# Optimization experiments

Hardware: AMD Instinct MI355X
Metric: run time of the kernel (lower is better)

The kernel has to match this reference:

```python
import jax, jax.numpy as jnp
import numpy as np

M_, N_, L_, K_ = 8, 64, 4, 4
PT = 10.0
B_ = 512
CH = 128
FLAT = 64 * M_ * (N_ + 1)  # PhaseNet flatten size


def setup_inputs() -> dict:
    key = jax.random.key(0)
    ks = jax.random.split(key, 25)
    rn = lambda k, shape, s=1.0: jax.random.normal(k, shape, jnp.float32) * s
    W_SCALE = 0.05
    return {
        "x": rn(ks[0], (B_, L_, 2 * K_, M_, N_ + 1)),
        "H_re": rn(ks[1], (B_, M_, N_, L_, K_)),
        "H_im": rn(ks[2], (B_, M_, N_, L_, K_)),
        "ch_re": rn(ks[3], (B_, K_, M_)),
        "ch_im": rn(ks[4], (B_, K_, M_)),
        # PhaseNet params (1x1 convs stored as [out, in])
        "conv1_w": rn(ks[5], (64, 2 * K_), W_SCALE), "conv1_b": jnp.zeros((64,), jnp.float32),
        "conv2_w": rn(ks[6], (64, 64), W_SCALE), "conv2_b": jnp.zeros((64,), jnp.float32),
        "pl1_w": rn(ks[7], (4 * N_, FLAT), W_SCALE), "pl1_b": jnp.zeros((4 * N_,), jnp.float32),
        "pl2_w": rn(ks[8], (2 * N_, 4 * N_), W_SCALE), "pl2_b": jnp.zeros((2 * N_,), jnp.float32),
        # BeamNet params
        "b1_w": rn(ks[9], (CH, 2 * K_ * M_), W_SCALE), "b1_b": jnp.zeros((CH,), jnp.float32),
        "b2_w": rn(ks[10], (CH, CH), W_SCALE), "b2_b": jnp.zeros((CH,), jnp.float32),
        "b3_w": rn(ks[11], (2 * M_ * (K_ + 1), CH), W_SCALE), "b3_b": jnp.zeros((2 * M_ * (K_ + 1),), jnp.float32),
        # powerNet params
        "p1_w": rn(ks[12], (CH, 2 * K_ * M_), W_SCALE), "p1_b": jnp.zeros((CH,), jnp.float32),
        "p2_w": rn(ks[13], (2, CH), W_SCALE), "p2_b": jnp.zeros((2,), jnp.float32),
    }


def reference(x, H_re, H_im, ch_re, ch_im,
              conv1_w, conv1_b, conv2_w, conv2_b, pl1_w, pl1_b, pl2_w, pl2_b,
              b1_w, b1_b, b2_w, b2_b, b3_w, b3_b, p1_w, p1_b, p2_w, p2_b):
    B = x.shape[0]
    # PhaseNet, batched over all L slices at once (1x1 convs == channel einsum)
    h = jax.nn.relu(jnp.einsum('blcmn,oc->blomn', x, conv1_w) + conv1_b[:, None, None])
    h = jax.nn.relu(jnp.einsum('blcmn,oc->blomn', h, conv2_w) + conv2_b[:, None, None])
    h = h.reshape(B, L_, FLAT)  # torch Flatten order (C, H, W) matches [o, m, n]
    h = jax.nn.relu(h @ pl1_w.T + pl1_b)
    Rl = h @ pl2_w.T + pl2_b  # [B, L, 2N]
    pr, pi = Rl[..., :N_], Rl[..., N_:]
    norm = jnp.maximum(jnp.sqrt(pr * pr + pi * pi), 1e-12)  # F.normalize over (re, im)
    Theta = jnp.stack([pr / norm, pi / norm], axis=-1)  # [B, L, N, 2]
    tr, ti = Theta[..., 0], Theta[..., 1]  # [B, L, N]
    # block-matrix [Re,Im;-Im,Re] @ [tr;ti], summed over l, for all k at once
    top = jnp.einsum('bmnlk,bln->bkm', H_re, tr) + jnp.einsum('bmnlk,bln->bkm', H_im, ti)
    bot = jnp.einsum('bmnlk,bln->bkm', H_re, ti) - jnp.einsum('bmnlk,bln->bkm', H_im, tr)
    concat_H = jnp.concatenate([top + ch_re, bot + ch_im], axis=-1).reshape(B, -1)  # [B, 2KM]
    # BeamNet
    W = jax.nn.relu(concat_H @ b1_w.T + b1_b)
    W = jax.nn.relu(W @ b2_w.T + b2_b)
    W = W @ b3_w.T + b3_b  # [B, 2M(K+1)]
    # powerNet
    mu = jax.nn.relu(concat_H @ p1_w.T + p1_b) @ p2_w.T + p2_b
    mu = jax.nn.softmax(mu, axis=1)  # [B, 2]
    Wn = jnp.maximum(jnp.linalg.norm(W, axis=1, keepdims=True), 1e-12)
    W = W / Wn * np.float32(np.sqrt(PT)) * jnp.sqrt(mu[:, :1])
    W = W.reshape(B, K_ + 1, 2 * M_)
    return W, Theta, mu
```

## Files before the change

kernel.cpp:

```cpp
#include <hip/hip_runtime.h>

#define ROWS 2048
#define FLATK 33280
#define CHUNK_K 16640
#define SUBK 2080
#define NSTEP 65
#define S_DIM 520
#define SPLITP 16
#define OUT_THETA 40960
#define OUT_MU 303104
#define LOSCALE 2048.0f
#define INV_LOSCALE (1.0f/2048.0f)

typedef __attribute__((ext_vector_type(8))) _Float16 f16x8;
typedef __attribute__((ext_vector_type(8))) unsigned short u16x8;
typedef __attribute__((ext_vector_type(4))) float f32x4;

union H16 { _Float16 h; unsigned short u; };

static __device__ __forceinline__ void split16(float v, unsigned short& hi, unsigned short& lo) {
    H16 a, b;
    a.h = (_Float16)v;
    float r = (v - (float)a.h) * LOSCALE;
    b.h = (_Float16)r;
    hi = a.u; lo = b.u;
}

static __device__ __forceinline__ void glds16(const unsigned short* g, unsigned short* l) {
    __builtin_amdgcn_global_load_lds((const __attribute__((address_space(1))) unsigned int*)g,
                                     (__attribute__((address_space(3))) unsigned int*)l,
                                     16, 0, 0);
}

__global__ __launch_bounds__(256) void k_cvtB(const float4* __restrict__ in,
                                              ushort4* __restrict__ outh,
                                              ushort4* __restrict__ outl, int n4) {
    int i = blockIdx.x * 256 + threadIdx.x;
    if (i >= n4) return;
    float4 v = in[i];
    unsigned short h0, h1, h2, h3, l0, l1, l2, l3;
    split16(v.x, h0, l0); split16(v.y, h1, l1);
    split16(v.z, h2, l2); split16(v.w, h3, l3);
    outh[i] = make_ushort4(h0, h1, h2, h3);
    outl[i] = make_ushort4(l0, l1, l2, l3);
}

__global__ __launch_bounds__(256) void k_cvtW(const float* __restrict__ w2,
                                              unsigned short* __restrict__ Wq) {
    int t = threadIdx.x;
    for (int s = t; s < 512; s += 256) {
        int z = s >> 8, rem = s & 255;
        int ot = rem >> 7, ks = (rem >> 6) & 1, lane = rem & 63;
        int m = lane & 15, kg = lane >> 4;
        const float* wp = w2 + (size_t)(z * 32 + ot * 16 + m) * 64 + ks * 32 + kg * 8;
#pragma unroll
        for (int j = 0; j < 8; j++) {
            unsigned short hh, ll;
            split16(wp[j], hh, ll);
            Wq[s * 8 + j] = hh;
            Wq[4096 + s * 8 + j] = ll;
        }
    }
}

__global__ __launch_bounds__(256) void k_conv(const float* __restrict__ x,
                                              const float* __restrict__ w1, const float* __restrict__ b1,
                                              const unsigned short* __restrict__ Wq,
                                              const float* __restrict__ b2,
                                              unsigned short* __restrict__ Ah, unsigned short* __restrict__ Al,
                                              int z) {
    __shared__ __align__(16) float xs[8 * 64];
    __shared__ __align__(16) float w1s[512];
    __shared__ float b1s[64];
    __shared__ __align__(16) unsigned short h1h[64 * 64];
    __shared__ __align__(16) unsigned short h1l[64 * 64];

    int t = threadIdx.x;
    int bl = blockIdx.x, st = blockIdx.y;
    int pbase = st * 64;
    int obase = z * 32;
    int lane = t & 63, w = t >> 6;
    int m = lane & 15, kg = lane >> 4;

    const float* xb = x + (size_t)bl * (8 * S_DIM);
    for (int i = t; i < 512; i += 256) {
        int ci = i >> 6, p = i & 63;
        int g = pbase + p;
        xs[i] = (g < S_DIM) ? xb[ci * S_DIM + g] : 0.f;
        w1s[i] = w1[i];
    }
    if (t < 64) b1s[t] = b1[t];

    f16x8 wh[2][2], wl[2][2];
    float b2v[2];
#pragma unroll
    for (int ot = 0; ot < 2; ot++) {
        b2v[ot] = b2[obase + ot * 16 + m];
#pragma unroll
        for (int ks = 0; ks < 2; ks++) {
            int slot = ((z * 2 + ot) * 2 + ks) * 64 + lane;
            wh[ot][ks] = *(const f16x8*)&Wq[slot * 8];
            wl[ot][ks] = *(const f16x8*)&Wq[4096 + slot * 8];
        }
    }
    __syncthreads();

    {
        int pos = lane;
        int cg0 = w * 16;
        float xv[8];
#pragma unroll
        for (int ci = 0; ci < 8; ci++) xv[ci] = xs[ci * 64 + pos];
#pragma unroll
        for (int half = 0; half < 2; half++) {
            u16x8 ph, pl;
#pragma unroll
            for (int j = 0; j < 8; j++) {
                int c = cg0 + half * 8 + j;
                const float4 wa = *(const float4*)&w1s[c * 8];
                const float4 wb = *(const float4*)&w1s[c * 8 + 4];
                float a = b1s[c]
                    + wa.x * xv[0] + wa.y * xv[1] + wa.z * xv[2] + wa.w * xv[3]
                    + wb.x * xv[4] + wb.y * xv[5] + wb.z * xv[6] + wb.w * xv[7];
                a = fmaxf(a, 0.f);
                unsigned short hh, ll;
                split16(a, hh, ll);
                ph[j] = hh; pl[j] = ll;
            }
            int g = (cg0 >> 3) + half;
            int off = pos * 64 + ((g ^ (pos & 7)) << 3);
            *(u16x8*)&h1h[off] = ph;
            *(u16x8*)&h1l[off] = pl;
        }
    }
    __syncthreads();

    int p0 = w * 16;
    int prow = p0 + m;
    f16x8 a_h[2], a_l[2];
#pragma unroll
    for (int ks = 0; ks < 2; ks++) {
        int g = ks * 4 + kg;
        int off = prow * 64 + ((g ^ (prow & 7)) << 3);
        a_h[ks] = *(const f16x8*)&h1h[off];
        a_l[ks] = *(const f16x8*)&h1l[off];
    }

    size_t Abase = (size_t)bl * CHUNK_K;
    int pos4 = pbase + p0 + kg * 4;
    bool ok = pos4 < (S_DIM - 3);
#pragma unroll
    for (int ot = 0; ot < 2; ot++) {
        f32x4 ah = {0.f, 0.f, 0.f, 0.f}, am = {0.f, 0.f, 0.f, 0.f};
#pragma unroll
        for (int ks = 0; ks < 2; ks++) {
            ah = __builtin_amdgcn_mfma_f32_16x16x32_f16(a_h[ks], wh[ot][ks], ah, 0, 0, 0);
            am = __builtin_amdgcn_mfma_f32_16x16x32_f16(a_l[ks], wh[ot][ks], am, 0, 0, 0);
            am = __builtin_amdgcn_mfma_f32_16x16x32_f16(a_h[ks], wl[ot][ks], am, 0, 0, 0);
        }
        if (ok) {
            unsigned short hh[4], ll[4];
#pragma unroll
            for (int r = 0; r < 4; r++) {
                float v = fmaxf(b2v[ot] + ah[r] + am[r] * INV_LOSCALE, 0.f);
                split16(v, hh[r], ll[r]);
            }
            size_t off2 = Abase + (size_t)(ot * 16 + m) * S_DIM + pos4;
            *reinterpret_cast<ushort4*>(&Ah[off2]) = make_ushort4(hh[0], hh[1], hh[2], hh[3]);
            *reinterpret_cast<ushort4*>(&Al[off2]) = make_ushort4(ll[0], ll[1], ll[2], ll[3]);
        }
    }
}

__global__ __launch_bounds__(256) void k_gemm(const unsigned short* __restrict__ Ah,
                                              const unsigned short* __restrict__ Al,
                                              const unsigned short* __restrict__ Bh,
                                              const unsigned short* __restrict__ Bl,
                                              float* __restrict__ P, int z) {
    __shared__ __align__(16) unsigned short As_h[64 * 32];
    __shared__ __align__(16) unsigned short As_l[64 * 32];
    __shared__ __align__(16) unsigned short Bs_h[128 * 32];
    __shared__ __align__(16) unsigned short Bs_l[128 * 32];

    int t = threadIdx.x;
    int rt = blockIdx.x, ct = blockIdx.y, sk = blockIdx.z;
    int row0 = rt * 64, col0 = ct * 128;
    int kb0 = sk * SUBK;

    int w = t >> 6, lane = t & 63;
    int srow = lane >> 2;
    int sg = (lane & 3) * 8;

    const unsigned short* gAh0 = Ah + (size_t)(row0 + w * 16 + srow) * CHUNK_K + kb0 + sg;
    const unsigned short* gAl0 = Al + (size_t)(row0 + w * 16 + srow) * CHUNK_K + kb0 + sg;
    const unsigned short* gBh0 = Bh + (size_t)(col0 + w * 32 + srow) * FLATK + (size_t)z * CHUNK_K + kb0 + sg;
    const unsigned short* gBl0 = Bl + (size_t)(col0 + w * 32 + srow) * FLATK + (size_t)z * CHUNK_K + kb0 + sg;
    const size_t strideB16 = (size_t)16 * FLATK;
    unsigned short* lAh  = &As_h[(w * 16) * 32];
    unsigned short* lAl  = &As_l[(w * 16) * 32];
    unsigned short* lBh0 = &Bs_h[(w * 32) * 32];
    unsigned short* lBh1 = &Bs_h[(w * 32 + 16) * 32];
    unsigned short* lBl0 = &Bs_l[(w * 32) * 32];
    unsigned short* lBl1 = &Bs_l[(w * 32 + 16) * 32];

    int m = lane & 15, kg = lane >> 4;

    f32x4 acc_h[4][2], acc_m[4][2];
#pragma unroll
    for (int i = 0; i < 4; i++)
#pragma unroll
        for (int j = 0; j < 2; j++) {
            acc_h[i][j] = (f32x4){0.f, 0.f, 0.f, 0.f};
            acc_m[i][j] = (f32x4){0.f, 0.f, 0.f, 0.f};
        }

    for (int it = 0; it < NSTEP; ++it) {
        __syncthreads();
        glds16(gAh0, lAh);
        glds16(gAl0, lAl);
        glds16(gBh0, lBh0);
        glds16(gBh0 + strideB16, lBh1);
        glds16(gBl0, lBl0);
        glds16(gBl0 + strideB16, lBl1);
        gAh0 += 32; gAl0 += 32; gBh0 += 32; gBl0 += 32;
        __syncthreads();

        f16x8 a_h[4], a_l[4], b_h[2], b_l[2];
#pragma unroll
        for (int i = 0; i < 4; i++) {
            int off = (i * 16 + m) * 32 + kg * 8;
            a_h[i] = *reinterpret_cast<const f16x8*>(&As_h[off]);
            a_l[i] = *reinterpret_cast<const f16x8*>(&As_l[off]);
        }
#pragma unroll
        for (int j = 0; j < 2; j++) {
            int off = (w * 32 + j * 16 + m) * 32 + kg * 8;
            b_h[j] = *reinterpret_cast<const f16x8*>(&Bs_h[off]);
            b_l[j] = *reinterpret_cast<const f16x8*>(&Bs_l[off]);
        }
#pragma unroll
        for (int i = 0; i < 4; i++)
#pragma unroll
            for (int j = 0; j < 2; j++) {
                acc_h[i][j] = __builtin_amdgcn_mfma_f32_16x16x32_f16(a_h[i], b_h[j], acc_h[i][j], 0, 0, 0);
                acc_m[i][j] = __builtin_amdgcn_mfma_f32_16x16x32_f16(a_l[i], b_h[j], acc_m[i][j], 0, 0, 0);
                acc_m[i][j] = __builtin_amdgcn_mfma_f32_16x16x32_f16(a_h[i], b_l[j], acc_m[i][j], 0, 0, 0);
            }
    }

    float* Pp = P + (size_t)(z * 8 + sk) * (ROWS * 256);
    int rbase = row0 + kg * 4;
    int cbase = col0 + w * 32 + m;
#pragma unroll
    for (int i = 0; i < 4; i++)
#pragma unroll
        for (int j = 0; j < 2; j++)
#pragma unroll
            for (int r = 0; r < 4; r++) {
                int rr = rbase + i * 16 + r;
                int cc = cbase + j * 16;
                Pp[(size_t)rr * 256 + cc] = acc_h[i][j][r] + acc_m[i][j][r] * INV_LOSCALE;
            }
}

__global__ __launch_bounds__(128) void k_head(const float* __restrict__ P,
                                              const float* __restrict__ pl1b,
                                              const float* __restrict__ pl2w,
                                              const float* __restrict__ pl2b,
                                              float* __restrict__ out) {
    __shared__ __align__(16) float hs[256];
    __shared__ float Rls[128];
    int row = blockIdx.x;
    int t = threadIdx.x;
    for (int c = t; c < 256; c += 128) {
        float v = pl1b[c];
#pragma unroll
        for (int zz = 0; zz < SPLITP; zz++) v += P[(size_t)zz * (ROWS * 256) + (size_t)row * 256 + c];
        hs[c] = fmaxf(v, 0.f);
    }
    __syncthreads();
    {
        float v = pl2b[t];
        const float4* wr = reinterpret_cast<const float4*>(pl2w + (size_t)t * 256);
        const float4* hv = reinterpret_cast<const float4*>(hs);
#pragma unroll 8
        for (int c4 = 0; c4 < 64; c4++) {
            float4 wq = wr[c4], h = hv[c4];
            v += wq.x * h.x + wq.y * h.y + wq.z * h.z + wq.w * h.w;
        }
        Rls[t] = v;
    }
    __syncthreads();
    if (t < 64) {
        float pr = Rls[t], pi = Rls[64 + t];
        float nrm = fmaxf(sqrtf(pr * pr + pi * pi), 1e-12f);
        float* th = out + OUT_THETA + (size_t)row * 128 + t * 2;
        th[0] = pr / nrm;
        th[1] = pi / nrm;
    }
}

__global__ __launch_bounds__(256) void k_tail(const float* __restrict__ Hre, const float* __restrict__ Him,
                                              const float* __restrict__ chre, const float* __restrict__ chim,
                                              const float* __restrict__ b1w, const float* __restrict__ b1b,
                                              const float* __restrict__ b2w, const float* __restrict__ b2b,
                                              const float* __restrict__ b3w, const float* __restrict__ b3b,
                                              const float* __restrict__ p1w, const float* __restrict__ p1b,
                                              const float* __restrict__ p2w, const float* __restrict__ p2b,
                                              float* __restrict__ out) {
    int b = blockIdx.x, t = threadIdx.x;
    __shared__ float trs[256], tis[256];
    __shared__ float red[512];
    __shared__ __align__(16) float cH[64];
    __shared__ __align__(16) float u1[128];
    __shared__ __align__(16) float u2[128];
    __shared__ __align__(16) float q1[128];
    __shared__ float wv[80];
    __shared__ float sc[4];

    const float* th = out + OUT_THETA + (size_t)b * 512;
    for (int i = t; i < 256; i += 256) { trs[i] = th[2 * i]; tis[i] = th[2 * i + 1]; }
    __syncthreads();

    {
        int part = t >> 5, km = t & 31, k = km >> 3, m = km & 7;
        const float* hr = Hre + (size_t)b * 8192 + m * 1024 + k;
        const float* hi = Him + (size_t)b * 8192 + m * 1024 + k;
        float a1 = 0.f, a2 = 0.f;
        for (int n = part * 8; n < part * 8 + 8; n++) {
#pragma unroll
            for (int l = 0; l < 4; l++) {
                float re = hr[n * 16 + l * 4], im = hi[n * 16 + l * 4];
                float tr = trs[l * 64 + n], ti = tis[l * 64 + n];
                a1 += re * tr + im * ti;
                a2 += re * ti - im * tr;
            }
        }
        red[(part * 32 + km) * 2 + 0] = a1;
        red[(part * 32 + km) * 2 + 1] = a2;
    }
    __syncthreads();
    if (t < 32) {
        float top = 0.f, bot = 0.f;
#pragma unroll
        for (int p = 0; p < 8; p++) { top += red[(p * 32 + t) * 2]; bot += red[(p * 32 + t) * 2 + 1]; }
        int k2 = t >> 3, m2 = t & 7;
        cH[k2 * 16 + m2]     = top + chre[b * 32 + t];
        cH[k2 * 16 + 8 + m2] = bot + chim[b * 32 + t];
    }
    __syncthreads();

    const float4* ch4 = reinterpret_cast<const float4*>(cH);
    if (t < 128) {
        float v = b1b[t];
        const float4* wq = reinterpret_cast<const float4*>(b1w + (size_t)t * 64);
#pragma unroll
        for (int j = 0; j < 16; j++) {
            float4 a = wq[j], c = ch4[j];
            v += a.x * c.x + a.y * c.y + a.z * c.z + a.w * c.w;
        }
        u1[t] = fmaxf(v, 0.f);
    } else {
        int o = t - 128;
        float v = p1b[o];
        const float4* wq = reinterpret_cast<const float4*>(p1w + (size_t)o * 64);
#pragma unroll
        for (int j = 0; j < 16; j++) {
            float4 a = wq[j], c = ch4[j];
            v += a.x * c.x + a.y * c.y + a.z * c.z + a.w * c.w;
        }
        q1[o] = fmaxf(v, 0.f);
    }
    __syncthreads();

    if (t < 128) {
        float v = b2b[t];
        const float4* wq = reinterpret_cast<const float4*>(b2w + (size_t)t * 128);
        const float4* uu = reinterpret_cast<const float4*>(u1);
#pragma unroll
        for (int j = 0; j < 32; j++) {
            float4 a = wq[j], c = uu[j];
            v += a.x * c.x + a.y * c.y + a.z * c.z + a.w * c.w;
        }
        u2[t] = fmaxf(v, 0.f);
    } else if (t < 130) {
        int o = t - 128;
        float v = p2b[o];
        const float4* wq = reinterpret_cast<const float4*>(p2w + (size_t)o * 128);
        const float4* qq = reinterpret_cast<const float4*>(q1);
#pragma unroll
        for (int j = 0; j < 32; j++) {
            float4 a = wq[j], c = qq[j];
            v += a.x * c.x + a.y * c.y + a.z * c.z + a.w * c.w;
        }
        sc[o] = v;
    }
    __syncthreads();

    if (t < 80) {
        float v = b3b[t];
        const float4* wq = reinterpret_cast<const float4*>(b3w + (size_t)t * 128);
        const float4* uu = reinterpret_cast<const float4*>(u2);
#pragma unroll
        for (int j = 0; j < 32; j++) {
            float4 a = wq[j], c = uu[j];
            v += a.x * c.x + a.y * c.y + a.z * c.z + a.w * c.w;
        }
        wv[t] = v;
    }
    __syncthreads();

    if (t == 0) {
        float mx = fmaxf(sc[0], sc[1]);
        float e0 = expf(sc[0] - mx), e1 = expf(sc[1] - mx);
        float s = e0 + e1;
        float mu0 = e0 / s, mu1 = e1 / s;
        out[OUT_MU + b * 2]     = mu0;
        out[OUT_MU + b * 2 + 1] = mu1;
        float ss = 0.f;
        for (int j = 0; j < 80; j++) ss += wv[j] * wv[j];
        float wn = fmaxf(sqrtf(ss), 1e-12f);
        sc[2] = 3.16227766017f * sqrtf(mu0) / wn;
    }
    __syncthreads();
    if (t < 80) out[b * 80 + t] = wv[t] * sc[2];
}

extern "C" void kernel_launch(void* const* d_in, const int* in_sizes, int n_in,
                              void* d_out, int out_size, void* d_ws, size_t ws_size,
                              hipStream_t stream) {
    const float* x    = (const float*)d_in[0];
    const float* Hre  = (const float*)d_in[1];
    const float* Him  = (const float*)d_in[2];
    const float* chre = (const float*)d_in[3];
    const float* chim = (const float*)d_in[4];
    const float* c1w  = (const float*)d_in[5];
    const float* c1b  = (const float*)d_in[6];
    const float* c2w  = (const float*)d_in[7];
    const float* c2b  = (const float*)d_in[8];
    const float* pl1w = (const float*)d_in[9];
    const float* pl1b = (const float*)d_in[10];
    const float* pl2w = (const float*)d_in[11];
    const float* pl2b = (const float*)d_in[12];
    const float* b1w  = (const float*)d_in[13];
    const float* b1b  = (const float*)d_in[14];
    const float* b2w  = (const float*)d_in[15];
    const float* b2b  = (const float*)d_in[16];
    const float* b3w  = (const float*)d_in[17];
    const float* b3b  = (const float*)d_in[18];
    const float* p1w  = (const float*)d_in[19];
    const float* p1b  = (const float*)d_in[20];
    const float* p2w  = (const float*)d_in[21];
    const float* p2b  = (const float*)d_in[22];
    float* out = (float*)d_out;

    char* ws = (char*)d_ws;
    unsigned short* Ah = (unsigned short*)(ws + 0);
    unsigned short* Al = (unsigned short*)(ws + 68157440u);
    float* P           = (float*)(ws + 136314880u);
    unsigned short* Bh = (unsigned short*)(ws + 169869312u);
    unsigned short* Bl = (unsigned short*)(ws + 186908672u);
    unsigned short* Wq = (unsigned short*)(ws + 169869312u - 16384u);

    k_cvtW<<<1, 256, 0, stream>>>(c2w, Wq);
    k_cvtB<<<8320, 256, 0, stream>>>((const float4*)pl1w, (ushort4*)Bh, (ushort4*)Bl, 2129920);
    for (int z = 0; z < 2; z++) {
        k_conv<<<dim3(2048, 9), 256, 0, stream>>>(x, c1w, c1b, Wq, c2b, Ah, Al, z);
        k_gemm<<<dim3(32, 2, 8), 256, 0, stream>>>(Ah, Al, Bh, Bl, P, z);
    }
    k_head<<<2048, 128, 0, stream>>>(P, pl1b, pl2w, pl2b, out);
    k_tail<<<512, 256, 0, stream>>>(Hre, Him, chre, chim, b1w, b1b, b2w, b2b,
                                    b3w, b3b, p1w, p1b, p2w, p2b, out);
}
```

Measured before the change: 524.1 us.

## Double-buffer LDS tiles in split-K GEMM to overlap loads with MFMA

Doubles the shared-memory A/B hi/lo tiles and issues the next k-step's global-to-LDS loads before computing on the current buffer. This leaves one barrier per iteration instead of two. The aim is to hide global load latency behind the MFMA work. In exchange it doubles LDS use per block, which may lower occupancy, and it depends on the barrier waiting for the async loads to finish.

```diff
diff --git a/kernel.cpp b/kernel.cpp
--- a/kernel.cpp
+++ b/kernel.cpp
@@ -177,10 +177,10 @@
                                               const unsigned short* __restrict__ Bh,
                                               const unsigned short* __restrict__ Bl,
                                               float* __restrict__ P, int z) {
-    __shared__ __align__(16) unsigned short As_h[64 * 32];
-    __shared__ __align__(16) unsigned short As_l[64 * 32];
-    __shared__ __align__(16) unsigned short Bs_h[128 * 32];
-    __shared__ __align__(16) unsigned short Bs_l[128 * 32];
+    __shared__ __align__(16) unsigned short As_h[2][64 * 32];
+    __shared__ __align__(16) unsigned short As_l[2][64 * 32];
+    __shared__ __align__(16) unsigned short Bs_h[2][128 * 32];
+    __shared__ __align__(16) unsigned short Bs_l[2][128 * 32];
 
     int t = threadIdx.x;
     int rt = blockIdx.x, ct = blockIdx.y, sk = blockIdx.z;
@@ -196,12 +196,9 @@
     const unsigned short* gBh0 = Bh + (size_t)(col0 + w * 32 + srow) * FLATK + (size_t)z * CHUNK_K + kb0 + sg;
     const unsigned short* gBl0 = Bl + (size_t)(col0 + w * 32 + srow) * FLATK + (size_t)z * CHUNK_K + kb0 + sg;
     const size_t strideB16 = (size_t)16 * FLATK;
-    unsigned short* lAh  = &As_h[(w * 16) * 32];
-    unsigned short* lAl  = &As_l[(w * 16) * 32];
-    unsigned short* lBh0 = &Bs_h[(w * 32) * 32];
-    unsigned short* lBh1 = &Bs_h[(w * 32 + 16) * 32];
-    unsigned short* lBl0 = &Bs_l[(w * 32) * 32];
-    unsigned short* lBl1 = &Bs_l[(w * 32 + 16) * 32];
+    int aoff = (w * 16) * 32;
+    int boff0 = (w * 32) * 32;
+    int boff1 = (w * 32 + 16) * 32;
 
     int m = lane & 15, kg = lane >> 4;
 
@@ -214,39 +211,54 @@
             acc_m[i][j] = (f32x4){0.f, 0.f, 0.f, 0.f};
         }
 
-    for (int it = 0; it < NSTEP; ++it) {
+#define STAGE(c) do {                                   \
+        glds16(gAh0, &As_h[c][aoff]);                   \
+        glds16(gAl0, &As_l[c][aoff]);                   \
+        glds16(gBh0, &Bs_h[c][boff0]);                  \
+        glds16(gBh0 + strideB16, &Bs_h[c][boff1]);      \
+        glds16(gBl0, &Bs_l[c][boff0]);                  \
+        glds16(gBl0 + strideB16, &Bs_l[c][boff1]);      \
+        gAh0 += 32; gAl0 += 32; gBh0 += 32; gBl0 += 32; \
+    } while (0)
+
+#define COMPUTE(c) do {                                                                   \
+        f16x8 a_h[4], a_l[4], b_h[2], b_l[2];                                             \
+        _Pragma("unroll")                                                                 \
+        for (int i = 0; i < 4; i++) {                                                     \
+            int off = (i * 16 + m) * 32 + kg * 8;                                         \
+            a_h[i] = *reinterpret_cast<const f16x8*>(&As_h[c][off]);                      \
+            a_l[i] = *reinterpret_cast<const f16x8*>(&As_l[c][off]);                      \
+        }                                                                                 \
+        _Pragma("unroll")                                                                 \
+        for (int j = 0; j < 2; j++) {                                                     \
+            int off = (w * 32 + j * 16 + m) * 32 + kg * 8;                                \
+            b_h[j] = *reinterpret_cast<const f16x8*>(&Bs_h[c][off]);                      \
+            b_l[j] = *reinterpret_cast<const f16x8*>(&Bs_l[c][off]);                      \
+        }                                                                                 \
+        _Pragma("unroll")                                                                 \
+        for (int i = 0; i < 4; i++)                                                       \
+            _Pragma("unroll")                                                             \
+            for (int j = 0; j < 2; j++) {                                                 \
+                acc_h[i][j] = __builtin_amdgcn_mfma_f32_16x16x32_f16(a_h[i], b_h[j], acc_h[i][j], 0, 0, 0); \
+                acc_m[i][j] = __builtin_amdgcn_mfma_f32_16x16x32_f16(a_l[i], b_h[j], acc_m[i][j], 0, 0, 0); \
+                acc_m[i][j] = __builtin_amdgcn_mfma_f32_16x16x32_f16(a_h[i], b_l[j], acc_m[i][j], 0, 0, 0); \
+            }                                                                             \
+    } while (0)
+
+    STAGE(0);
+    __syncthreads();
+
+    int cur = 0;
+    for (int it = 0; it < NSTEP - 1; ++it) {
+        STAGE(cur ^ 1);
+        COMPUTE(cur);
         __syncthreads();
-        glds16(gAh0, lAh);
-        glds16(gAl0, lAl);
-        glds16(gBh0, lBh0);
-        glds16(gBh0 + strideB16, lBh1);
-        glds16(gBl0, lBl0);
-        glds16(gBl0 + strideB16, lBl1);
-        gAh0 += 32; gAl0 += 32; gBh0 += 32; gBl0 += 32;
-        __syncthreads();
-
-        f16x8 a_h[4], a_l[4], b_h[2], b_l[2];
-#pragma unroll
-        for (int i = 0; i < 4; i++) {
-            int off = (i * 16 + m) * 32 + kg * 8;
-            a_h[i] = *reinterpret_cast<const f16x8*>(&As_h[off]);
-            a_l[i] = *reinterpret_cast<const f16x8*>(&As_l[off]);
-        }
-#pragma unroll
-        for (int j = 0; j < 2; j++) {
-            int off = (w * 32 + j * 16 + m) * 32 + kg * 8;
-            b_h[j] = *reinterpret_cast<const f16x8*>(&Bs_h[off]);
-            b_l[j] = *reinterpret_cast<const f16x8*>(&Bs_l[off]);
-        }
-#pragma unroll
-        for (int i = 0; i < 4; i++)
-#pragma unroll
-            for (int j = 0; j < 2; j++) {
-                acc_h[i][j] = __builtin_amdgcn_mfma_f32_16x16x32_f16(a_h[i], b_h[j], acc_h[i][j], 0, 0, 0);
-                acc_m[i][j] = __builtin_amdgcn_mfma_f32_16x16x32_f16(a_l[i], b_h[j], acc_m[i][j], 0, 0, 0);
-                acc_m[i][j] = __builtin_amdgcn_mfma_f32_16x16x32_f16(a_h[i], b_l[j], acc_m[i][j], 0, 0, 0);
-            }
-    }
+        cur ^= 1;
+    }
+    COMPUTE(cur);
+
+#undef STAGE
+#undef COMPUTE
 
     float* Pp = P + (size_t)(z * 8 + sk) * (ROWS * 256);
     int rbase = row0 + kg * 4;
```

New measurement: 537.4 us. +2.5%, slower.
